# Performance work log

Hardware: AMD Instinct MI355X
Metric: run time of the kernel (lower is better)

Reference implementation:

```python
import jax, jax.numpy as jnp
import numpy as np

N_NEIGHBORS = 9
NOISE_MIN, NOISE_MAX = 0.01, 0.5
EPS = 1e-8


def setup_inputs() -> dict:
    key = jax.random.key(0)
    k1, k2 = jax.random.split(key)
    features = jax.random.normal(k1, (8, 1024, 28, 28), dtype=jnp.float32)
    memory_bank = jax.random.normal(k2, (16384, 1024), dtype=jnp.float32)
    return {"features": features, "memory_bank": memory_bank}


def _knn_influence(f, memory_bank):
    # f: [N, C], memory_bank: [M, C]
    # squared euclidean distances via norm + matmul (same math as torch batched loop)
    d2 = (
        jnp.sum(f * f, axis=1, keepdims=True)
        + jnp.sum(memory_bank * memory_bank, axis=1)[None, :]
        - 2.0 * (f @ memory_bank.T)
    )  # [N, M]
    dist = jnp.sqrt(jnp.clip(d2, 0.0) + EPS)
    neg_top, idx = jax.lax.top_k(-dist, N_NEIGHBORS)  # smallest-K, ascending
    knn_dist = -neg_top  # [N, K]
    nearest = memory_bank[idx[:, 0]]  # [N, C]
    grad = (f - nearest) / (knn_dist[:, 0:1] + EPS)
    influence = jnp.abs(grad).mean(axis=1)  # [N]
    return influence, knn_dist


def reference(features, memory_bank):
    B, C, H, W = features.shape
    f = jnp.transpose(features, (0, 2, 3, 1)).reshape(-1, C)  # [N, C]
    influence, _ = _knn_influence(f, memory_bank)
    imin, imax = influence.min(), influence.max()
    influence_norm = jnp.where(imax - imin > EPS, (influence - imin) / (imax - imin), jnp.zeros_like(influence))
    noise_std = NOISE_MIN + influence_norm * (NOISE_MAX - NOISE_MIN)  # [N]
    noise = jax.random.normal(jax.random.key(1), f.shape, dtype=f.dtype) * noise_std[:, None]
    noised = (f + noise).reshape(B, H, W, C).transpose(0, 3, 1, 2)
    return noised, influence_norm.reshape(B, H, W), noise_std.reshape(B, H, W)
```

## Files before the change

kernel.cpp:

```cpp
#include <hip/hip_runtime.h>
#include <float.h>
#include <math.h>

#define M_ROWS 6272
#define N_BANK 16384
#define K_DIM  1024
#define HW     784
#define CHW    802816
#define OUT_NORM_OFF 6422528
#define OUT_STD_OFF  6428800
#define N_ELEMS 6422528

#define DELTA 0.5f
#define JSPLIT 32
#define JCHUNK (N_BANK / JSPLIT)
#define CAP 1024

#define WS_SIDX 0
#define WS_INFL 8192
#define WS_MM   20736
#define WS_MBN  20744
#define WS_PB   40960
#define WS_PS   241664
#define WS_PI   442368
#define WS_LIST 643072
#define WS_RPV  644096
#define WS_RPI  775168

typedef __attribute__((ext_vector_type(8))) short bf16x8;
typedef __attribute__((ext_vector_type(4))) float f32x4;

__device__ __forceinline__ unsigned rotl32(unsigned v, int r){ return (v << r) | (v >> (32 - r)); }

__device__ __forceinline__ void tf2x32(unsigned k0, unsigned k1, unsigned x0, unsigned x1,
                                       unsigned& o0, unsigned& o1){
  const unsigned ks2 = k0 ^ k1 ^ 0x1BD11BDAu;
  x0 += k0; x1 += k1;
#define TF_ROUND(rot) { x0 += x1; x1 = rotl32(x1, rot); x1 ^= x0; }
  TF_ROUND(13) TF_ROUND(15) TF_ROUND(26) TF_ROUND(6)
  x0 += k1;  x1 += ks2 + 1u;
  TF_ROUND(17) TF_ROUND(29) TF_ROUND(16) TF_ROUND(24)
  x0 += ks2; x1 += k0 + 2u;
  TF_ROUND(13) TF_ROUND(15) TF_ROUND(26) TF_ROUND(6)
  x0 += k0;  x1 += k1 + 3u;
  TF_ROUND(17) TF_ROUND(29) TF_ROUND(16) TF_ROUND(24)
  x0 += k1;  x1 += ks2 + 4u;
  TF_ROUND(13) TF_ROUND(15) TF_ROUND(26) TF_ROUND(6)
  x0 += ks2; x1 += k0 + 5u;
#undef TF_ROUND
  o0 = x0; o1 = x1;
}

__device__ __forceinline__ float normal_from_bits(unsigned bits){
  unsigned fb = (bits >> 9) | 0x3F800000u;
  float f = __uint_as_float(fb) - 1.0f;
  const float lo = __uint_as_float(0xBF7FFFFFu);
  float u = fmaxf(lo, f * 2.0f + lo);
  float w = -log1pf(-u * u);
  float p;
  if (w < 5.0f){
    w = w - 2.5f;
    p = 2.81022636e-08f;
    p = fmaf(p, w, 3.43273939e-07f);
    p = fmaf(p, w, -3.5233877e-06f);
    p = fmaf(p, w, -4.39150654e-06f);
    p = fmaf(p, w, 0.00021858087f);
    p = fmaf(p, w, -0.00125372503f);
    p = fmaf(p, w, -0.00417768164f);
    p = fmaf(p, w, 0.246640727f);
    p = fmaf(p, w, 1.50140941f);
  } else {
    w = sqrtf(w) - 3.0f;
    p = -0.000200214257f;
    p = fmaf(p, w, 0.000100950558f);
    p = fmaf(p, w, 0.00134934322f);
    p = fmaf(p, w, -0.00367342844f);
    p = fmaf(p, w, 0.00573950773f);
    p = fmaf(p, w, -0.0076224613f);
    p = fmaf(p, w, 0.00943887047f);
    p = fmaf(p, w, 1.00167406f);
    p = fmaf(p, w, 2.83297682f);
  }
  return 1.41421356237f * (p * u);
}

__device__ __forceinline__ unsigned f2bf(float x){
  unsigned u = __float_as_uint(x);
  return (u + 0x7FFFu + ((u >> 16) & 1u)) >> 16;
}

__global__ __launch_bounds__(256) void mbnorm_kernel(const float* __restrict__ mb, float* __restrict__ mbn){
  int wid  = (blockIdx.x * 256 + threadIdx.x) >> 6;
  int lane = threadIdx.x & 63;
  if (wid >= N_BANK) return;
  const float* row = mb + (size_t)wid * K_DIM;
  float s = 0.f;
#pragma unroll
  for (int i = 0; i < 16; ++i){ float v = row[lane + i*64]; s = fmaf(v, v, s); }
#pragma unroll
  for (int off = 32; off; off >>= 1) s += __shfl_down(s, off);
  if (lane == 0) mbn[wid] = s;
}

__global__ void init_kernel(int* __restrict__ cnt){ if (threadIdx.x == 0) *cnt = 0; }

__global__ __launch_bounds__(256) void knn_min_kernel(
    const float* __restrict__ feat, const float* __restrict__ mb,
    const float* __restrict__ mbn,
    float* __restrict__ pbest, float* __restrict__ psec, int* __restrict__ pidx)
{
  __shared__ __align__(16) unsigned short As[8192];
  __shared__ __align__(16) unsigned short Bs[8192];

  const int t    = threadIdx.x;
  const int lane = t & 63;
  const int w    = t >> 6;
  const int wr   = w >> 1, wc = w & 1;
  const int lrow = lane >> 4;
  const int lcol = lane & 15;
  const int r0   = blockIdx.x * 128;
  const int j0base = blockIdx.y * JCHUNK;

  const int sIdx  = t & 127;
  const int oBase = t >> 7;
  const int rowA  = r0 + sIdx;
  const int bA    = rowA / HW;
  const int baseA = bA * CHW + (rowA - bA * HW);
  const int sSw   = sIdx & 7;

  float best[16], sec[16]; int bidx[16];
#pragma unroll
  for (int i = 0; i < 16; ++i){ best[i] = FLT_MAX; sec[i] = FLT_MAX; bidx[i] = 0; }

  for (int panel = 0; panel < JCHUNK/128; ++panel){
    const int j0 = j0base + panel*128;
    f32x4 acc[4][4];
#pragma unroll
    for (int mi = 0; mi < 4; ++mi)
#pragma unroll
      for (int ni = 0; ni < 4; ++ni) acc[mi][ni] = (f32x4){0.f,0.f,0.f,0.f};

    for (int k0 = 0; k0 < K_DIM; k0 += 64){
      __syncthreads();
#pragma unroll
      for (int ii = 0; ii < 4; ++ii){
        const int octet = oBase + 2*ii;
        const int kb = k0 + octet*8;
        float x0 = feat[baseA + (kb+0)*HW];
        float x1 = feat[baseA + (kb+1)*HW];
        float x2 = feat[baseA + (kb+2)*HW];
        float x3 = feat[baseA + (kb+3)*HW];
        float x4 = feat[baseA + (kb+4)*HW];
        float x5 = feat[baseA + (kb+5)*HW];
        float x6 = feat[baseA + (kb+6)*HW];
        float x7 = feat[baseA + (kb+7)*HW];
        uint4 q;
        q.x = f2bf(x0) | (f2bf(x1) << 16);
        q.y = f2bf(x2) | (f2bf(x3) << 16);
        q.z = f2bf(x4) | (f2bf(x5) << 16);
        q.w = f2bf(x6) | (f2bf(x7) << 16);
        ((uint4*)As)[sIdx*8 + (octet ^ sSw)] = q;
      }
#pragma unroll
      for (int ii = 0; ii < 4; ++ii){
        const int octet = oBase + 2*ii;
        const float* src = mb + (size_t)(j0 + sIdx) * K_DIM + k0 + octet*8;
        const float4 v0 = *reinterpret_cast<const float4*>(src);
        const float4 v1 = *reinterpret_cast<const float4*>(src + 4);
        uint4 q;
        q.x = f2bf(v0.x) | (f2bf(v0.y) << 16);
        q.y = f2bf(v0.z) | (f2bf(v0.w) << 16);
        q.z = f2bf(v1.x) | (f2bf(v1.y) << 16);
        q.w = f2bf(v1.z) | (f2bf(v1.w) << 16);
        ((uint4*)Bs)[sIdx*8 + (octet ^ sSw)] = q;
      }
      __syncthreads();
#pragma unroll
      for (int kk = 0; kk < 2; ++kk){
        const int oct = kk*4 + lrow;
        bf16x8 av[4], bv[4];
#pragma unroll
        for (int mi = 0; mi < 4; ++mi){
          int idx = (wr*4 + mi)*16 + lcol;
          av[mi] = *reinterpret_cast<const bf16x8*>(&As[idx*64 + ((oct ^ (lcol & 7)) << 3)]);
        }
#pragma unroll
        for (int ni = 0; ni < 4; ++ni){
          int idx = (wc*4 + ni)*16 + lcol;
          bv[ni] = *reinterpret_cast<const bf16x8*>(&Bs[idx*64 + ((oct ^ (lcol & 7)) << 3)]);
        }
#pragma unroll
        for (int mi = 0; mi < 4; ++mi)
#pragma unroll
          for (int ni = 0; ni < 4; ++ni)
            acc[mi][ni] = __builtin_amdgcn_mfma_f32_16x16x32_bf16(av[mi], bv[ni], acc[mi][ni], 0, 0, 0);
      }
    }

#pragma unroll
    for (int ni = 0; ni < 4; ++ni){
      int j = j0 + wc*64 + ni*16 + lcol;
      float mv = mbn[j];
#pragma unroll
      for (int mi = 0; mi < 4; ++mi)
#pragma unroll
        for (int rg = 0; rg < 4; ++rg){
          float s = fmaf(-2.0f, acc[mi][ni][rg], mv);
          int st = mi*4 + rg;
          if (s < best[st]){ sec[st] = best[st]; best[st] = s; bidx[st] = j; }
          else if (s < sec[st]){ sec[st] = s; }
        }
    }
  }

#pragma unroll
  for (int st = 0; st < 16; ++st){
    float b = best[st], s2 = sec[st]; int ix = bidx[st];
#pragma unroll
    for (int m = 1; m < 16; m <<= 1){
      float ob = __shfl_xor(b, m);
      float os = __shfl_xor(s2, m);
      int   oi = __shfl_xor(ix, m);
      if (ob < b || (ob == b && oi < ix)){ s2 = fminf(os, b); b = ob; ix = oi; }
      else { s2 = fminf(s2, ob); }
    }
    best[st] = b; sec[st] = s2; bidx[st] = ix;
  }

  __syncthreads();
  float* rb  = (float*)As;
  float* rsv = rb + 256;
  int*   rix = (int*)(rsv + 256);
  if (lcol == 0){
#pragma unroll
    for (int st = 0; st < 16; ++st){
      int rloc = wr*64 + (st>>2)*16 + lrow*4 + (st&3);
      rb [rloc*2 + wc] = best[st];
      rsv[rloc*2 + wc] = sec[st];
      rix[rloc*2 + wc] = bidx[st];
    }
  }
  __syncthreads();
  if (t < 128){
    float b0 = rb[t*2], s0 = rsv[t*2]; int i0 = rix[t*2];
    float b1 = rb[t*2+1], s1 = rsv[t*2+1]; int i1 = rix[t*2+1];
    float gb, gs; int gi;
    if (b1 < b0 || (b1 == b0 && i1 < i0)){ gb = b1; gi = i1; gs = fminf(s1, b0); }
    else { gb = b0; gi = i0; gs = fminf(s0, b1); }
    pbest[blockIdx.y * M_ROWS + r0 + t] = gb;
    psec [blockIdx.y * M_ROWS + r0 + t] = gs;
    pidx [blockIdx.y * M_ROWS + r0 + t] = gi;
  }
}

__global__ __launch_bounds__(256) void reduce_parts_kernel(
    const float* __restrict__ pbest, const float* __restrict__ psec, const int* __restrict__ pidx,
    int* __restrict__ sidx, int* __restrict__ list, int* __restrict__ cnt)
{
  int r = blockIdx.x * blockDim.x + threadIdx.x;
  if (r >= M_ROWS) return;
  float gb = FLT_MAX, gs = FLT_MAX; int gi = 0;
#pragma unroll
  for (int p = 0; p < JSPLIT; ++p){
    float v = pbest[p * M_ROWS + r], s2 = psec[p * M_ROWS + r]; int ii = pidx[p * M_ROWS + r];
    if (v < gb || (v == gb && ii < gi)){ gs = fminf(gb, s2); gb = v; gi = ii; }
    else { gs = fminf(gs, v); }
  }
  sidx[r] = gi;
  if (gs - gb < DELTA){
    int pos = atomicAdd(cnt, 1);
    if (pos < CAP) list[pos] = r;
  }
}

__global__ __launch_bounds__(256) void refine_part_kernel(
    const float* __restrict__ feat, const float* __restrict__ mb,
    const int* __restrict__ list, const int* __restrict__ cnt,
    double* __restrict__ rpv, int* __restrict__ rpi)
{
  __shared__ float fs[K_DIM];
  __shared__ double wvv[4]; __shared__ int wvi[4];
  const int nf = min(*cnt, CAP);
  const int nwork = nf * 64;
  const int wv = threadIdx.x >> 6, lane = threadIdx.x & 63;

  for (int w = blockIdx.x; w < nwork; w += gridDim.x){
    const int fi = w >> 6, chunk = w & 63;
    const int r = list[fi];
    const int b = r / HW, hw = r - b * HW;
    for (int c = threadIdx.x; c < K_DIM; c += 256) fs[c] = feat[b * CHW + c * HW + hw];
    __syncthreads();

    double bv = DBL_MAX; int bi = N_BANK;
    for (int rr = 0; rr < 64; ++rr){
      int j = chunk * 256 + wv * 64 + rr;
      const float* mrow = mb + (size_t)j * K_DIM;
      double s = 0.0;
#pragma unroll
      for (int i = 0; i < 16; ++i){
        int c = lane + i * 64;
        double d = (double)fs[c] - (double)mrow[c];
        s = fma(d, d, s);
      }
#pragma unroll
      for (int off = 1; off < 64; off <<= 1) s += __shfl_xor(s, off);
      if (s < bv){ bv = s; bi = j; }
    }
    if (lane == 0){ wvv[wv] = bv; wvi[wv] = bi; }
    __syncthreads();
    if (threadIdx.x == 0){
      double gv = wvv[0]; int gi2 = wvi[0];
#pragma unroll
      for (int x = 1; x < 4; ++x){
        if (wvv[x] < gv || (wvv[x] == gv && wvi[x] < gi2)){ gv = wvv[x]; gi2 = wvi[x]; }
      }
      rpv[fi * 64 + chunk] = gv; rpi[fi * 64 + chunk] = gi2;
    }
    __syncthreads();
  }
}

__global__ __launch_bounds__(256) void refine_combine_kernel(
    const double* __restrict__ rpv, const int* __restrict__ rpi,
    const int* __restrict__ list, const int* __restrict__ cnt, int* __restrict__ sidx)
{
  const int nf = min(*cnt, CAP);
  const int wv = threadIdx.x >> 6, lane = threadIdx.x & 63;
  for (int fi = wv; fi < nf; fi += 4){
    double v = rpv[fi * 64 + lane]; int ii = rpi[fi * 64 + lane];
#pragma unroll
    for (int off = 1; off < 64; off <<= 1){
      double ov = __shfl_xor(v, off); int oi = __shfl_xor(ii, off);
      if (ov < v || (ov == v && oi < ii)){ v = ov; ii = oi; }
    }
    if (lane == 0) sidx[list[fi]] = ii;
  }
}

__global__ __launch_bounds__(256) void influence_kernel(
    const float* __restrict__ feat, const float* __restrict__ mb,
    const int* __restrict__ sidx, double* __restrict__ infl)
{
  const int wid  = (blockIdx.x * 256 + threadIdx.x) >> 6;
  const int lane = threadIdx.x & 63;
  if (wid >= M_ROWS) return;
  const int r = wid;
  const int b = r / HW;
  const int baseR = b * CHW + (r - b * HW);
  const float* mrow = mb + (size_t)sidx[r] * K_DIM;
  double sabs = 0.0, sd2 = 0.0;
#pragma unroll
  for (int i = 0; i < 16; ++i){
    int c = lane + i*64;
    double d = (double)feat[baseR + c * HW] - (double)mrow[c];
    sd2  = fma(d, d, sd2);
    sabs += fabs(d);
  }
#pragma unroll
  for (int off = 1; off < 64; off <<= 1){
    sabs += __shfl_xor(sabs, off);
    sd2  += __shfl_xor(sd2, off);
  }
  if (lane == 0){
    double dist = sqrt(fmax(sd2, 0.0) + 1e-8);
    infl[r] = (sabs / 1024.0) / (dist + 1e-8);
  }
}

__global__ __launch_bounds__(1024) void minmax_kernel(const double* __restrict__ infl, double* __restrict__ mm){
  __shared__ double smn[1024], smx[1024];
  int t = threadIdx.x;
  double mn = DBL_MAX, mx = -DBL_MAX;
  for (int i = t; i < M_ROWS; i += 1024){ double v = infl[i]; mn = fmin(mn, v); mx = fmax(mx, v); }
  smn[t] = mn; smx[t] = mx; __syncthreads();
  for (int off = 512; off > 0; off >>= 1){
    if (t < off){ smn[t] = fmin(smn[t], smn[t+off]); smx[t] = fmax(smx[t], smx[t+off]); }
    __syncthreads();
  }
  if (t == 0){ mm[0] = smn[0]; mm[1] = smx[0]; }
}

__global__ __launch_bounds__(256) void normstd_kernel(
    const double* __restrict__ mm, const double* __restrict__ infl,
    float* __restrict__ norm_out, float* __restrict__ std_out, double* __restrict__ dws)
{
  int r = blockIdx.x * blockDim.x + threadIdx.x;
  if (r >= M_ROWS) return;
  double imin = mm[0], imax = mm[1];
  if (r == 0){ dws[0] = imin; dws[1] = imax; }
  double rng = imax - imin;
  double nrm = (rng > 1e-8) ? (infl[r] - imin) / rng : 0.0;
  norm_out[r] = (float)nrm;
  std_out[r]  = (float)(0.01 + nrm * 0.49);
}

__global__ __launch_bounds__(256) void noise_kernel(
    const float* __restrict__ feat, const float* __restrict__ stds, float* __restrict__ out)
{
  int tid = blockIdx.x * 256 + threadIdx.x;
  int b   = tid / CHW;
  int rem = tid - b * CHW;
  int c   = rem / HW;
  int hw  = rem - c * HW;
  int r   = b * HW + hw;
  unsigned e = (unsigned)r * (unsigned)K_DIM + (unsigned)c;
  unsigned o0, o1;
  tf2x32(0u, 1u, 0u, e, o0, o1);
  unsigned bits = o0 ^ o1;
  float n = normal_from_bits(bits);
  out[tid] = feat[tid] + n * stds[r];
}

__global__ void diag_kernel(const double* __restrict__ dws, float* __restrict__ out){
  double imin = dws[0], imax = dws[1];
  double rng = imax - imin;
  double code = 0.0, payload = 0.0;
  if (!(imin == imin) || !(imax == imax)){ code = 5e6; }
  else if (rng <= 1e-8){ code = 1e6; payload = fmin(fmax(rng, 0.0) * 1e12, 9e5); }
  else if (imax > 0.5){ code = 2e6; payload = fmin(imax * 1e4, 9e5); }
  else if (imin <= 1e-4){ code = 3e6; payload = fmin(fmax(imin, 0.0) * 1e6, 9e5); }
  else if (imax > 10.0 * imin){ code = 4e6; payload = fmin(imax * 1e4, 9e5); }
  if (code > 0.0) out[0] = (float)(code + payload);
}

__global__ void kat_kernel(float* __restrict__ out){
  float code = 0.f;
  unsigned a, b;
  tf2x32(0u, 0u, 0u, 0u, a, b);
  if (a != 0x6b200159u || b != 0x99ba4efeu) code = 1e10f;
  unsigned c2, d2;
  tf2x32(0x13198a2eu, 0x03707344u, 0x243f6a88u, 0x85a308d3u, c2, d2);
  if (code == 0.f && (c2 != 0xc4923a9cu || d2 != 0x483df7a0u)) code = 3e9f;
  float n = normal_from_bits(0x6b200159u);
  if (code == 0.f && fabsf(n - (-0.20584226f)) > 2e-5f) code = 1e9f;
  if (code > 0.f) out[0] = code;
}

extern "C" void kernel_launch(void* const* d_in, const int* in_sizes, int n_in,
                              void* d_out, int out_size, void* d_ws, size_t ws_size,
                              hipStream_t stream) {
  const float* feat = (const float*)d_in[0];
  const float* mb   = (const float*)d_in[1];
  float* out = (float*)d_out;

  int*    sidx = (int*)(out + WS_SIDX);
  double* infl = (double*)(out + WS_INFL);
  double* mm   = (double*)(out + WS_MM);
  float*  mbn  = out + WS_MBN;
  float*  pb   = out + WS_PB;
  float*  ps   = out + WS_PS;
  int*    pi   = (int*)(out + WS_PI);
  int*    list = (int*)(out + WS_LIST);
  double* rpv  = (double*)(out + WS_RPV);
  int*    rpi  = (int*)(out + WS_RPI);
  double* dws  = (double*)d_ws;
  int*    cnt  = (int*)((char*)d_ws + 16);
  float*  nrm  = out + OUT_NORM_OFF;
  float*  stds = out + OUT_STD_OFF;

  mbnorm_kernel<<<N_BANK/4, 256, 0, stream>>>(mb, mbn);
  init_kernel<<<1, 64, 0, stream>>>(cnt);
  knn_min_kernel<<<dim3(M_ROWS/128, JSPLIT), 256, 0, stream>>>(feat, mb, mbn, pb, ps, pi);
  reduce_parts_kernel<<<(M_ROWS + 255)/256, 256, 0, stream>>>(pb, ps, pi, sidx, list, cnt);
  refine_part_kernel<<<2048, 256, 0, stream>>>(feat, mb, list, cnt, rpv, rpi);
  refine_combine_kernel<<<1, 256, 0, stream>>>(rpv, rpi, list, cnt, sidx);
  influence_kernel<<<(M_ROWS*64)/256, 256, 0, stream>>>(feat, mb, sidx, infl);
  minmax_kernel<<<1, 1024, 0, stream>>>(infl, mm);
  normstd_kernel<<<(M_ROWS + 255)/256, 256, 0, stream>>>(mm, infl, nrm, stds, dws);
  noise_kernel<<<N_ELEMS/256, 256, 0, stream>>>(feat, stds, out);
  diag_kernel<<<1, 1, 0, stream>>>(dws, out);
  kat_kernel<<<1, 1, 0, stream>>>(out);
}
```

Before: 2.112 ms.

## Pre-transpose features to bf16 and register-prefetch next tile in knn GEMM

Adds a kernel that transposes the NCHW features into a row-major bf16 buffer stored in the output region, so the knn GEMM loads A as contiguous 16-byte vectors instead of eight strided scalar loads with conversion. The knn loop is flattened into a single 64-step loop over panels and k-steps, and global loads for the next step are issued into registers before the MFMA work on the current step, overlapping memory latency with compute. This costs an extra transpose pass and more registers, which may lower occupancy, and the bf16 buffer overlaps output memory that is later overwritten.

```diff
diff --git a/kernel.cpp b/kernel.cpp
--- a/kernel.cpp
+++ b/kernel.cpp
@@ -26,6 +26,7 @@
 #define WS_LIST 643072
 #define WS_RPV  644096
 #define WS_RPI  775168
+#define WS_FBF  1048576
 
 typedef __attribute__((ext_vector_type(8))) short bf16x8;
 typedef __attribute__((ext_vector_type(4))) float f32x4;
@@ -104,8 +105,31 @@
 
 __global__ void init_kernel(int* __restrict__ cnt){ if (threadIdx.x == 0) *cnt = 0; }
 
+__global__ __launch_bounds__(256) void featbf_kernel(const float* __restrict__ feat,
+                                                     unsigned short* __restrict__ fbf){
+  __shared__ unsigned short tile[128][18];
+  const int b   = blockIdx.z;
+  const int hw0 = blockIdx.x * 16;
+  const int c0  = blockIdx.y * 128;
+  const int t   = threadIdx.x;
+  const int hw_l = t & 15, c_l = t >> 4;
+#pragma unroll
+  for (int i = 0; i < 8; ++i){
+    int c = c_l + 16*i;
+    float v = feat[b*CHW + (c0 + c)*HW + hw0 + hw_l];
+    tile[c][hw_l] = (unsigned short)f2bf(v);
+  }
+  __syncthreads();
+  const int c_w = t & 127, hw_b = t >> 7;
+#pragma unroll
+  for (int i = 0; i < 8; ++i){
+    int hw_w = hw_b + 2*i;
+    fbf[(size_t)(b*HW + hw0 + hw_w)*K_DIM + c0 + c_w] = tile[c_w][hw_w];
+  }
+}
+
 __global__ __launch_bounds__(256) void knn_min_kernel(
-    const float* __restrict__ feat, const float* __restrict__ mb,
+    const unsigned short* __restrict__ fbf, const float* __restrict__ mb,
     const float* __restrict__ mbn,
     float* __restrict__ pbest, float* __restrict__ psec, int* __restrict__ pidx)
 {
@@ -121,95 +145,95 @@
   const int r0   = blockIdx.x * 128;
   const int j0base = blockIdx.y * JCHUNK;
 
-  const int sIdx  = t & 127;
-  const int oBase = t >> 7;
-  const int rowA  = r0 + sIdx;
-  const int bA    = rowA / HW;
-  const int baseA = bA * CHW + (rowA - bA * HW);
-  const int sSw   = sIdx & 7;
+  uint4  ra[4];
+  float4 rb0[4], rb1[4];
 
   float best[16], sec[16]; int bidx[16];
 #pragma unroll
   for (int i = 0; i < 16; ++i){ best[i] = FLT_MAX; sec[i] = FLT_MAX; bidx[i] = 0; }
 
-  for (int panel = 0; panel < JCHUNK/128; ++panel){
-    const int j0 = j0base + panel*128;
-    f32x4 acc[4][4];
-#pragma unroll
-    for (int mi = 0; mi < 4; ++mi)
-#pragma unroll
-      for (int ni = 0; ni < 4; ++ni) acc[mi][ni] = (f32x4){0.f,0.f,0.f,0.f};
-
-    for (int k0 = 0; k0 < K_DIM; k0 += 64){
-      __syncthreads();
+  f32x4 acc[4][4];
+
+#pragma unroll
+  for (int ii = 0; ii < 4; ++ii){
+    int id = t + 256*ii; int idx = id >> 3, oct = id & 7;
+    ra[ii] = *reinterpret_cast<const uint4*>(&fbf[(size_t)(r0 + idx)*K_DIM + oct*8]);
+    const float* src = mb + (size_t)(j0base + idx)*K_DIM + oct*8;
+    rb0[ii] = *reinterpret_cast<const float4*>(src);
+    rb1[ii] = *reinterpret_cast<const float4*>(src + 4);
+  }
+
+  for (int s = 0; s < 64; ++s){
+    const int panel = s >> 4;
+    const int kstep = s & 15;
+    if (kstep == 0){
+#pragma unroll
+      for (int mi = 0; mi < 4; ++mi)
+#pragma unroll
+        for (int ni = 0; ni < 4; ++ni) acc[mi][ni] = (f32x4){0.f,0.f,0.f,0.f};
+    }
+    __syncthreads();
+#pragma unroll
+    for (int ii = 0; ii < 4; ++ii){
+      int id = t + 256*ii; int idx = id >> 3, oct = id & 7;
+      ((uint4*)As)[idx*8 + (oct ^ (idx & 7))] = ra[ii];
+      uint4 q;
+      q.x = f2bf(rb0[ii].x) | (f2bf(rb0[ii].y) << 16);
+      q.y = f2bf(rb0[ii].z) | (f2bf(rb0[ii].w) << 16);
+      q.z = f2bf(rb1[ii].x) | (f2bf(rb1[ii].y) << 16);
+      q.w = f2bf(rb1[ii].z) | (f2bf(rb1[ii].w) << 16);
+      ((uint4*)Bs)[idx*8 + (oct ^ (idx & 7))] = q;
+    }
+    __syncthreads();
+    if (s < 63){
+      const int s2 = s + 1;
+      const int k0n = (s2 & 15) * 64;
+      const int j0n = j0base + (s2 >> 4) * 128;
 #pragma unroll
       for (int ii = 0; ii < 4; ++ii){
-        const int octet = oBase + 2*ii;
-        const int kb = k0 + octet*8;
-        float x0 = feat[baseA + (kb+0)*HW];
-        float x1 = feat[baseA + (kb+1)*HW];
-        float x2 = feat[baseA + (kb+2)*HW];
-        float x3 = feat[baseA + (kb+3)*HW];
-        float x4 = feat[baseA + (kb+4)*HW];
-        float x5 = feat[baseA + (kb+5)*HW];
-        float x6 = feat[baseA + (kb+6)*HW];
-        float x7 = feat[baseA + (kb+7)*HW];
-        uint4 q;
-        q.x = f2bf(x0) | (f2bf(x1) << 16);
-        q.y = f2bf(x2) | (f2bf(x3) << 16);
-        q.z = f2bf(x4) | (f2bf(x5) << 16);
-        q.w = f2bf(x6) | (f2bf(x7) << 16);
-        ((uint4*)As)[sIdx*8 + (octet ^ sSw)] = q;
-      }
-#pragma unroll
-      for (int ii = 0; ii < 4; ++ii){
-        const int octet = oBase + 2*ii;
-        const float* src = mb + (size_t)(j0 + sIdx) * K_DIM + k0 + octet*8;
-        const float4 v0 = *reinterpret_cast<const float4*>(src);
-        const float4 v1 = *reinterpret_cast<const float4*>(src + 4);
-        uint4 q;
-        q.x = f2bf(v0.x) | (f2bf(v0.y) << 16);
-        q.y = f2bf(v0.z) | (f2bf(v0.w) << 16);
-        q.z = f2bf(v1.x) | (f2bf(v1.y) << 16);
-        q.w = f2bf(v1.z) | (f2bf(v1.w) << 16);
-        ((uint4*)Bs)[sIdx*8 + (octet ^ sSw)] = q;
-      }
-      __syncthreads();
-#pragma unroll
-      for (int kk = 0; kk < 2; ++kk){
-        const int oct = kk*4 + lrow;
-        bf16x8 av[4], bv[4];
-#pragma unroll
-        for (int mi = 0; mi < 4; ++mi){
-          int idx = (wr*4 + mi)*16 + lcol;
-          av[mi] = *reinterpret_cast<const bf16x8*>(&As[idx*64 + ((oct ^ (lcol & 7)) << 3)]);
-        }
-#pragma unroll
-        for (int ni = 0; ni < 4; ++ni){
-          int idx = (wc*4 + ni)*16 + lcol;
-          bv[ni] = *reinterpret_cast<const bf16x8*>(&Bs[idx*64 + ((oct ^ (lcol & 7)) << 3)]);
-        }
+        int id = t + 256*ii; int idx = id >> 3, oct = id & 7;
+        ra[ii] = *reinterpret_cast<const uint4*>(&fbf[(size_t)(r0 + idx)*K_DIM + k0n + oct*8]);
+        const float* src = mb + (size_t)(j0n + idx)*K_DIM + k0n + oct*8;
+        rb0[ii] = *reinterpret_cast<const float4*>(src);
+        rb1[ii] = *reinterpret_cast<const float4*>(src + 4);
+      }
+    }
+#pragma unroll
+    for (int kk = 0; kk < 2; ++kk){
+      const int oct = kk*4 + lrow;
+      bf16x8 av[4], bv[4];
+#pragma unroll
+      for (int mi = 0; mi < 4; ++mi){
+        int idx = (wr*4 + mi)*16 + lcol;
+        av[mi] = *reinterpret_cast<const bf16x8*>(&As[idx*64 + ((oct ^ (lcol & 7)) << 3)]);
+      }
+#pragma unroll
+      for (int ni = 0; ni < 4; ++ni){
+        int idx = (wc*4 + ni)*16 + lcol;
+        bv[ni] = *reinterpret_cast<const bf16x8*>(&Bs[idx*64 + ((oct ^ (lcol & 7)) << 3)]);
+      }
+#pragma unroll
+      for (int mi = 0; mi < 4; ++mi)
+#pragma unroll
+        for (int ni = 0; ni < 4; ++ni)
+          acc[mi][ni] = __builtin_amdgcn_mfma_f32_16x16x32_bf16(av[mi], bv[ni], acc[mi][ni], 0, 0, 0);
+    }
+    if (kstep == 15){
+      const int j0 = j0base + panel*128;
+#pragma unroll
+      for (int ni = 0; ni < 4; ++ni){
+        int j = j0 + wc*64 + ni*16 + lcol;
+        float mv = mbn[j];
 #pragma unroll
         for (int mi = 0; mi < 4; ++mi)
 #pragma unroll
-          for (int ni = 0; ni < 4; ++ni)
-            acc[mi][ni] = __builtin_amdgcn_mfma_f32_16x16x32_bf16(av[mi], bv[ni], acc[mi][ni], 0, 0, 0);
-      }
-    }
-
-#pragma unroll
-    for (int ni = 0; ni < 4; ++ni){
-      int j = j0 + wc*64 + ni*16 + lcol;
-      float mv = mbn[j];
-#pragma unroll
-      for (int mi = 0; mi < 4; ++mi)
-#pragma unroll
-        for (int rg = 0; rg < 4; ++rg){
-          float s = fmaf(-2.0f, acc[mi][ni][rg], mv);
-          int st = mi*4 + rg;
-          if (s < best[st]){ sec[st] = best[st]; best[st] = s; bidx[st] = j; }
-          else if (s < sec[st]){ sec[st] = s; }
-        }
+          for (int rg = 0; rg < 4; ++rg){
+            float sv = fmaf(-2.0f, acc[mi][ni][rg], mv);
+            int st = mi*4 + rg;
+            if (sv < best[st]){ sec[st] = best[st]; best[st] = sv; bidx[st] = j; }
+            else if (sv < sec[st]){ sec[st] = sv; }
+          }
+      }
     }
   }
 
@@ -453,6 +477,7 @@
   int*    list = (int*)(out + WS_LIST);
   double* rpv  = (double*)(out + WS_RPV);
   int*    rpi  = (int*)(out + WS_RPI);
+  unsigned short* fbf = (unsigned short*)(out + WS_FBF);
   double* dws  = (double*)d_ws;
   int*    cnt  = (int*)((char*)d_ws + 16);
   float*  nrm  = out + OUT_NORM_OFF;
@@ -460,7 +485,8 @@
 
   mbnorm_kernel<<<N_BANK/4, 256, 0, stream>>>(mb, mbn);
   init_kernel<<<1, 64, 0, stream>>>(cnt);
-  knn_min_kernel<<<dim3(M_ROWS/128, JSPLIT), 256, 0, stream>>>(feat, mb, mbn, pb, ps, pi);
+  featbf_kernel<<<dim3(49, 8, 8), 256, 0, stream>>>(feat, fbf);
+  knn_min_kernel<<<dim3(M_ROWS/128, JSPLIT), 256, 0, stream>>>(fbf, mb, mbn, pb, ps, pi);
   reduce_parts_kernel<<<(M_ROWS + 255)/256, 256, 0, stream>>>(pb, ps, pi, sidx, list, cnt);
   refine_part_kernel<<<2048, 256, 0, stream>>>(feat, mb, list, cnt, rpv, rpi);
   refine_combine_kernel<<<1, 256, 0, stream>>>(rpv, rpi, list, cnt, sidx);
```

New measurement: 1.879 ms. 11.0% less time.
